# Kernel tuning notes

Measured on AMD Instinct MI355X. Metric: run time of the kernel, lower is better.

The kernel has to match this reference:

```python
import jax, jax.numpy as jnp
import numpy as np
import math

LEVEL_DIMS = [256, 512, 1024, 2048]
B, P, K, D = 8192, 64, 8, 512
EPS = 1e-5  # torch LayerNorm default eps


def _layernorm(x, g, b):
    m = jnp.mean(x, axis=-1, keepdims=True)
    v = jnp.var(x, axis=-1, keepdims=True)
    return (x - m) / jnp.sqrt(v + EPS) * g + b


def _l2norm(x):
    # F.normalize(dim=-1): x / max(||x||_2, 1e-12)
    n = jnp.sqrt(jnp.sum(x * x, axis=-1, keepdims=True))
    return x / jnp.maximum(n, 1e-12)


def setup_inputs() -> dict:
    key = jax.random.key(0)
    ks = iter(jax.random.split(key, 32))
    inp = {}
    for i, dim in enumerate(LEVEL_DIMS):
        inp[f'pooled_{i}'] = jax.random.normal(next(ks), (B, dim), jnp.float32)
        inp[f'proto_{i}'] = jax.random.normal(next(ks), (P, dim), jnp.float32)
        inp[f'ln_g_{i}'] = jnp.ones((2 * dim,), jnp.float32)
        inp[f'ln_b_{i}'] = jnp.zeros((2 * dim,), jnp.float32)
        inp[f'W_{i}'] = jax.random.normal(next(ks), (2 * dim, D), jnp.float32) * (1.0 / math.sqrt(2 * dim))
        inp[f'b_{i}'] = jnp.zeros((D,), jnp.float32)
    inp['text_base'] = jax.random.normal(next(ks), (K, D), jnp.float32)
    inp['logit_scale'] = jnp.ones((1,), jnp.float32)
    return inp


def reference(pooled_0, pooled_1, pooled_2, pooled_3,
              proto_0, proto_1, proto_2, proto_3,
              ln_g_0, ln_g_1, ln_g_2, ln_g_3,
              ln_b_0, ln_b_1, ln_b_2, ln_b_3,
              W_0, W_1, W_2, W_3,
              b_0, b_1, b_2, b_3,
              text_base, logit_scale):
    pooled = [pooled_0, pooled_1, pooled_2, pooled_3]
    proto = [proto_0, proto_1, proto_2, proto_3]
    ln_g = [ln_g_0, ln_g_1, ln_g_2, ln_g_3]
    ln_b = [ln_b_0, ln_b_1, ln_b_2, ln_b_3]
    Ws = [W_0, W_1, W_2, W_3]
    bs = [b_0, b_1, b_2, b_3]

    # text encoder: CLIP embeddings normalized, text_proj=Identity, normalized again (idempotent)
    text_features = _l2norm(text_base)  # [K, D]

    ctxs = []
    for pl, pr, g, bb, W, b in zip(pooled, proto, ln_g, ln_b, Ws, bs):
        proto_ctx = jnp.broadcast_to(jnp.mean(pr, axis=0, keepdims=True), pl.shape)  # [B, C]
        fused = jnp.concatenate([pl, proto_ctx], axis=1)  # [B, 2C]
        h = jax.nn.relu(_layernorm(fused, g, bb) @ W + b)  # [B, D]
        ctxs.append(_l2norm(h))
    image_contexts = jnp.stack(ctxs, axis=1)  # [B, L, D]

    logits = jnp.einsum('kd,bld->bkl', text_features, image_contexts)
    logits = logits / math.sqrt(D)
    logits = logits * jnp.clip(logit_scale, 1e-4, None)
    return jax.nn.softmax(logits, axis=-1)  # [B, K, L]
```

## Files before the change

kernel.cpp:

```cpp
#include <hip/hip_runtime.h>
#include <stdint.h>

typedef __bf16 bf16x8 __attribute__((ext_vector_type(8)));
typedef float f32x4 __attribute__((ext_vector_type(4)));

#define OFF_ABF   0u
#define OFF_GWT   62914560u
#define OFF_H     66846720u
#define OFF_STAT  100401152u
#define OFF_TEXT  100663296u
#define OFF_U     100679680u
#define OFF_GG    100687872u
#define OFF_BB    100696064u
#define OFF_SCAL  100704256u
#define OFF_PMEAN 100704512u
#define WS_TOTAL  100719872u

__host__ __device__ __forceinline__ size_t abf_off(int l) {
  return (size_t)4194304u * (size_t)((1u << l) - 1u);
}
__host__ __device__ __forceinline__ size_t gwt_off(int l) {
  return (size_t)262144u * (size_t)((1u << l) - 1u);
}
__device__ __forceinline__ int pm_off(int l) { return 256 * ((1 << l) - 1); }

__device__ __forceinline__ unsigned short f2bf(float x) {
  return (unsigned short)((__float_as_uint(x) + 0x8000u) >> 16);
}
__device__ __forceinline__ unsigned pack2(float a, float b) {
  return ((__float_as_uint(a) + 0x8000u) >> 16) |
         ((__float_as_uint(b) + 0x8000u) & 0xffff0000u);
}
__device__ __forceinline__ void async_load16(const void* g, void* l) {
  __builtin_amdgcn_global_load_lds((const __attribute__((address_space(1))) void*)g,
                                   (__attribute__((address_space(3))) void*)l,
                                   16, 0, 0);
}

struct PrepArgs {
  const float* pooled[4];
  const float* proto[4];
  const float* W[4];
  const float* g[4];
  const float* beta[4];
  const float* bias[4];
  const float* text;
  const float* lsc;
  char* ws;
};


__device__ __forceinline__ void loadUnit(f32x4 (&buf)[8], const f32x4* base, int lane) {
#pragma unroll
  for (int i = 0; i < 4; ++i) {
    buf[2 * i]     = base[2 * (lane + 64 * i)];
    buf[2 * i + 1] = base[2 * (lane + 64 * i) + 1];
  }
}

template <int R>
__device__ __forceinline__ void procUnit(const f32x4 (&v)[8], char* Dst, float* st,
                                         int rowBase, int lane) {
  float p1[4], p2[4];
#pragma unroll
  for (int i = 0; i < 4; ++i) {
    f32x4 a = v[2 * i], b = v[2 * i + 1];
    float s1 = ((a[0] + a[1]) + (a[2] + a[3])) + ((b[0] + b[1]) + (b[2] + b[3]));
    float s2 = 0.f;
    s2 = fmaf(a[0], a[0], s2); s2 = fmaf(a[1], a[1], s2);
    s2 = fmaf(a[2], a[2], s2); s2 = fmaf(a[3], a[3], s2);
    s2 = fmaf(b[0], b[0], s2); s2 = fmaf(b[1], b[1], s2);
    s2 = fmaf(b[2], b[2], s2); s2 = fmaf(b[3], b[3], s2);
    p1[i] = s1; p2[i] = s2;
    uint4 o = make_uint4(pack2(a[0], a[1]), pack2(a[2], a[3]),
                         pack2(b[0], b[1]), pack2(b[2], b[3]));
    *(uint4*)(Dst + 16 * (size_t)(lane + 64 * i)) = o;
  }
  if constexpr (R == 1) {
    float s1 = (p1[0] + p1[1]) + (p1[2] + p1[3]);
    float s2 = (p2[0] + p2[1]) + (p2[2] + p2[3]);
#pragma unroll
    for (int off = 1; off < 64; off <<= 1) {
      s1 += __shfl_xor(s1, off); s2 += __shfl_xor(s2, off);
    }
    if (lane == 0) {
      st[2 * (size_t)rowBase] = s1; st[2 * (size_t)rowBase + 1] = s2;
    }
  } else if constexpr (R == 2) {
#pragma unroll
    for (int h = 0; h < 2; ++h) {
      float s1 = p1[2 * h] + p1[2 * h + 1], s2 = p2[2 * h] + p2[2 * h + 1];
#pragma unroll
      for (int off = 1; off < 64; off <<= 1) {
        s1 += __shfl_xor(s1, off); s2 += __shfl_xor(s2, off);
      }
      if (lane == 0) {
        st[2 * (size_t)(rowBase + h)] = s1; st[2 * (size_t)(rowBase + h) + 1] = s2;
      }
    }
  } else if constexpr (R == 4) {
#pragma unroll
    for (int i = 0; i < 4; ++i) {
      float s1 = p1[i], s2 = p2[i];
#pragma unroll
      for (int off = 1; off < 64; off <<= 1) {
        s1 += __shfl_xor(s1, off); s2 += __shfl_xor(s2, off);
      }
      if (lane == 0) {
        st[2 * (size_t)(rowBase + i)] = s1; st[2 * (size_t)(rowBase + i) + 1] = s2;
      }
    }
  } else {
#pragma unroll
    for (int i = 0; i < 4; ++i) {
      float s1 = p1[i], s2 = p2[i];
#pragma unroll
      for (int off = 1; off < 32; off <<= 1) {
        s1 += __shfl_xor(s1, off); s2 += __shfl_xor(s2, off);
      }
      if ((lane & 31) == 0) {
        int row = rowBase + 2 * i + (lane >> 5);
        st[2 * (size_t)row] = s1; st[2 * (size_t)row + 1] = s2;
      }
    }
  }
}

template <int R>
__device__ __forceinline__ void waveRun(const f32x4* P, char* Dst, float* st,
                                        int rowBase, int lane) {
  f32x4 bufA[8], bufB[8];
  loadUnit(bufA, P, lane);
#pragma unroll
  for (int k = 0; k < 8; ++k) {
    if ((k & 1) == 0) {
      if (k < 7) loadUnit(bufB, P + (size_t)(k + 1) * 512, lane);
      procUnit<R>(bufA, Dst + (size_t)k * 4096, st, rowBase + k * R, lane);
    } else {
      if (k < 7) loadUnit(bufA, P + (size_t)(k + 1) * 512, lane);
      procUnit<R>(bufB, Dst + (size_t)k * 4096, st, rowBase + k * R, lane);
    }
  }
}

__global__ __launch_bounds__(256, 4) void aconv(PrepArgs A) {
  __shared__ float redP[4][64];
  int t = threadIdx.x, bid = blockIdx.x;
  int w = t >> 6, lane = t & 63;

  if (bid < 480) {
    int u0 = (bid * 4 + w) * 8;
    int l, uL;
    if (u0 < 8192)       { l = 3; uL = u0; }
    else if (u0 < 12288) { l = 2; uL = u0 - 8192; }
    else if (u0 < 14336) { l = 1; uL = u0 - 12288; }
    else                 { l = 0; uL = u0 - 14336; }
    const f32x4* P = (const f32x4*)A.pooled[l] + (size_t)uL * 512;
    char* Dst = A.ws + OFF_ABF + abf_off(l) + (size_t)uL * 4096;
    float* st = (float*)(A.ws + OFF_STAT) + (size_t)l * 8192 * 2;
    if (l == 3)      waveRun<1>(P, Dst, st, uL,     lane);
    else if (l == 2) waveRun<2>(P, Dst, st, uL * 2, lane);
    else if (l == 1) waveRun<4>(P, Dst, st, uL * 4, lane);
    else             waveRun<8>(P, Dst, st, uL * 8, lane);
    return;
  }
  float* scal = (float*)(A.ws + OFF_SCAL);
  if (bid < 540) {
    int p = bid - 480;
    int l, chunk;
    if (p < 32)      { l = 3; chunk = p; }
    else if (p < 48) { l = 2; chunk = p - 32; }
    else if (p < 56) { l = 1; chunk = p - 48; }
    else             { l = 0; chunk = p - 56; }
    int C = 256 << l;
    int c = chunk * 64 + lane;
    const float* pr = A.proto[l];
    float s = 0.f;
#pragma unroll
    for (int r = 0; r < 16; ++r) s += pr[(size_t)(w * 16 + r) * C + c];
    redP[w][lane] = s;
    __syncthreads();
    if (t < 64) {
      float pmv = (redP[0][t] + redP[1][t] + redP[2][t] + redP[3][t]) * (1.0f / 64.0f);
      ((float*)(A.ws + OFF_PMEAN))[pm_off(l) + chunk * 64 + t] = pmv;
      float s1 = pmv, s2 = pmv * pmv;
#pragma unroll
      for (int off = 1; off < 64; off <<= 1) {
        s1 += __shfl_xor(s1, off);
        s2 += __shfl_xor(s2, off);
      }
      if (t == 0) {
        atomicAdd(&scal[l], s1);
        atomicAdd(&scal[4 + l], s2);
      }
    }
    return;
  }
  float* r1 = &redP[0][0];
  float* tf = (float*)(A.ws + OFF_TEXT);
  for (int r = 0; r < 8; ++r) {
    float p = 0.f;
    for (int c = t; c < 512; c += 256) {
      float v = A.text[r * 512 + c];
      p += v * v;
    }
    r1[t] = p;
    __syncthreads();
    for (int o = 128; o > 0; o >>= 1) {
      if (t < o) r1[t] += r1[t + o];
      __syncthreads();
    }
    float inv = 1.0f / fmaxf(sqrtf(r1[0]), 1e-12f);
    __syncthreads();
    for (int c = t; c < 512; c += 256) tf[r * 512 + c] = A.text[r * 512 + c] * inv;
  }
  if (t == 0) {
    float s = fmaxf(A.lsc[0], 1e-4f);
    scal[8] = s * 0.04419417382415922f;
  }
}

__global__ __launch_bounds__(256) void wtrans(PrepArgs A) {
  __shared__ unsigned short tile[128][66];
  __shared__ float redG[4][128], redB[4][128], redU[4][128];
  __shared__ float gsh[64], bsh[64], psh[64];
  int t = threadIdx.x, bid = blockIdx.x;
  int l, idl;
  if (bid < 256)      { l = 3; idl = bid; }
  else if (bid < 384) { l = 2; idl = bid - 256; }
  else if (bid < 448) { l = 1; idl = bid - 384; }
  else                { l = 0; idl = bid - 448; }
  int C = 256 << l;
  int sid = idl >> 2, dchunk = idl & 3;
  int j0 = sid * 64, d0 = dchunk * 128;
  bool top = (j0 < C);

  if (t < 64) {
    float gv = A.g[l][j0 + t];
    gsh[t] = gv;
    bsh[t] = A.beta[l][j0 + t];
    if (!top)
      psh[t] = ((const float*)(A.ws + OFF_PMEAN))[pm_off(l) + (j0 - C) + t] * gv;
  }
  __syncthreads();

  int w = t >> 6, L = t & 63;
  const float* W = A.W[l];
  float2 v[16];
#pragma unroll
  for (int r = 0; r < 16; ++r) {
    int j = j0 + w * 16 + r;
    v[r] = *(const float2*)(W + (size_t)j * 512 + d0 + 2 * L);
  }
  float gp0 = 0.f, gp1 = 0.f, bp0 = 0.f, bp1 = 0.f, up0 = 0.f, up1 = 0.f;
#pragma unroll
  for (int r = 0; r < 16; ++r) {
    int jl = w * 16 + r;
    float g = gsh[jl], b = bsh[jl];
    gp0 = fmaf(g, v[r].x, gp0); gp1 = fmaf(g, v[r].y, gp1);
    bp0 = fmaf(b, v[r].x, bp0); bp1 = fmaf(b, v[r].y, bp1);
    if (top) {
      tile[2 * L][jl] = f2bf(g * v[r].x);
      tile[2 * L + 1][jl] = f2bf(g * v[r].y);
    } else {
      float p = psh[jl];
      up0 = fmaf(p, v[r].x, up0); up1 = fmaf(p, v[r].y, up1);
    }
  }
  redG[w][2 * L] = gp0; redG[w][2 * L + 1] = gp1;
  redB[w][2 * L] = bp0; redB[w][2 * L + 1] = bp1;
  if (!top) { redU[w][2 * L] = up0; redU[w][2 * L + 1] = up1; }
  __syncthreads();

  if (t < 128) {
    int d = l * 512 + d0 + t;
    float G = redG[0][t] + redG[1][t] + redG[2][t] + redG[3][t];
    float B = redB[0][t] + redB[1][t] + redB[2][t] + redB[3][t];
    atomicAdd(&((float*)(A.ws + OFF_GG))[d], G);
    atomicAdd(&((float*)(A.ws + OFF_BB))[d], B);
    if (!top) {
      float U = redU[0][t] + redU[1][t] + redU[2][t] + redU[3][t];
      atomicAdd(&((float*)(A.ws + OFF_U))[d], U);
    }
  }
  if (top) {
    unsigned short* gwT = (unsigned short*)(A.ws + OFF_GWT + gwt_off(l));
    int d = t >> 1, jh = (t & 1) * 32;
    const unsigned* trow = (const unsigned*)&tile[d][jh];
    uint4 q0 = make_uint4(trow[0], trow[1], trow[2], trow[3]);
    uint4 q1 = make_uint4(trow[4], trow[5], trow[6], trow[7]);
    uint4 q2 = make_uint4(trow[8], trow[9], trow[10], trow[11]);
    uint4 q3 = make_uint4(trow[12], trow[13], trow[14], trow[15]);
    uint4* dst = (uint4*)(gwT + (size_t)(d0 + d) * C + j0 + jh);
    dst[0] = q0; dst[1] = q1; dst[2] = q2; dst[3] = q3;
  }
}

struct G2Args {
  char* ws;
  const float* bias[4];
};

__global__ __launch_bounds__(256, 3) void gemm2(G2Args A) {
  __shared__ __align__(16) char lds[18944];
  char* ws = A.ws;
  int t = threadIdx.x, bid = blockIdx.x;
  int l = 3 - (bid >> 8);
  int rb = (bid >> 2) & 63, cb = bid & 3;
  int C = 256 << l;
  int m0 = rb * 128, n0 = cb * 128;

  float* uArr  = (float*)(lds + 16384);
  float* gArr  = (float*)(lds + 16896);
  float* bArr  = (float*)(lds + 17408);
  float* rowM  = (float*)(lds + 17920);
  float* rowIS = (float*)(lds + 18432);
  const float* scal = (const float*)(ws + OFF_SCAL);

  if (t < 128) {
    int idx = l * 512 + n0 + t;
    uArr[t] = ((const float*)(ws + OFF_U))[idx];
    gArr[t] = ((const float*)(ws + OFF_GG))[idx];
    bArr[t] = ((const float*)(ws + OFF_BB))[idx] + A.bias[l][n0 + t];
  } else {
    int r = t - 128;
    const float* st = (const float*)(ws + OFF_STAT) + (size_t)(l * 8192 + m0 + r) * 2;
    float s1 = st[0], s2 = st[1];
    float inv2C = 1.0f / (float)(2 * C);
    float mr = (s1 + scal[l]) * inv2C;
    float var = (s2 + scal[4 + l]) * inv2C - mr * mr;
    rowM[r] = mr;
    rowIS[r] = rsqrtf(var + 1e-5f);
  }

  int w = t >> 6, lane = t & 63, quad = lane >> 4, lc = lane & 15;
  const char* Abf = ws + OFF_ABF + abf_off(l);
  const char* Bw  = ws + OFF_GWT + gwt_off(l);
  const char* aP[2]; const char* bP[2];
  char* aD[2]; char* bD[2];
#pragma unroll
  for (int i = 0; i < 2; ++i) {
    int li = i * 256 + t;
    int rr = li >> 2, kq = li & 3;
    aP[i] = Abf + ((size_t)(m0 + rr) * C + kq * 8) * 2;
    bP[i] = Bw  + ((size_t)(n0 + rr) * C + kq * 8) * 2;
    aD[i] = lds + i * 4096 + w * 1024;
    bD[i] = lds + 8192 + i * 4096 + w * 1024;
  }
  int wr = (w >> 1) * 64, wc = (w & 1) * 64;
  const char* aF = lds + (wr + lc) * 64 + quad * 16;
  const char* bF = lds + 8192 + (wc + lc) * 64 + quad * 16;

  f32x4 acc[4][4] = {};
  for (int k0 = 0; k0 < C; k0 += 32) {
    async_load16(aP[0], aD[0]); async_load16(aP[1], aD[1]);
    async_load16(bP[0], bD[0]); async_load16(bP[1], bD[1]);
    aP[0] += 64; aP[1] += 64; bP[0] += 64; bP[1] += 64;
    __syncthreads();
    bf16x8 av[4];
#pragma unroll
    for (int rt = 0; rt < 4; ++rt) av[rt] = *(const bf16x8*)(aF + rt * 1024);
#pragma unroll
    for (int ct = 0; ct < 4; ++ct) {
      bf16x8 bv = *(const bf16x8*)(bF + ct * 1024);
#pragma unroll
      for (int rt = 0; rt < 4; ++rt)
        acc[rt][ct] = __builtin_amdgcn_mfma_f32_16x16x32_bf16(av[rt], bv, acc[rt][ct], 0, 0, 0);
    }
    __syncthreads();
  }

  char* Hl = ws + OFF_H + (size_t)l * 8388608;
#pragma unroll
  for (int rt = 0; rt < 4; ++rt) {
#pragma unroll
    for (int ct = 0; ct < 4; ++ct) {
      int nl = wc + ct * 16 + lc;
      float uu = uArr[nl], gg = gArr[nl], bb = bArr[nl];
      f32x4 a = acc[rt][ct];
#pragma unroll
      for (int reg = 0; reg < 4; ++reg) {
        int ml = wr + rt * 16 + quad * 4 + reg;
        float h = fmaf(a[reg] + uu - rowM[ml] * gg, rowIS[ml], bb);
        h = fmaxf(h, 0.f);
        float hp = __shfl_xor(h, 1);
        if (!(lc & 1)) {
          unsigned pkv = pack2(h, hp);
          *(unsigned*)(Hl + ((size_t)(m0 + ml) * 512 + n0 + nl) * 2) = pkv;
        }
      }
    }
  }
}

__global__ __launch_bounds__(256) void postK(const char* ws, float* out) {
  __shared__ float textL[4096];
  int t = threadIdx.x, b = blockIdx.x;
  const float* tf = (const float*)(ws + OFF_TEXT);
  for (int i = t; i < 4096; i += 256) textL[i] = tf[i];
  __syncthreads();
  float scale = ((const float*)(ws + OFF_SCAL))[8];
  int row = b * 16 + (t >> 4), q = t & 15;
  float lg[4][8];
#pragma unroll
  for (int l = 0; l < 4; ++l) {
    const uint4* hp = (const uint4*)(ws + OFF_H + (size_t)l * 8388608 +
                                     ((size_t)row * 512 + q * 32) * 2);
    float np = 0.f;
    float dp[8] = {};
#pragma unroll
    for (int ch = 0; ch < 4; ++ch) {
      uint4 u = hp[ch];
      int d0 = q * 32 + ch * 8;
      unsigned uw[4] = {u.x, u.y, u.z, u.w};
#pragma unroll
      for (int p = 0; p < 4; ++p) {
        float v0 = __uint_as_float(uw[p] << 16);
        float v1 = __uint_as_float(uw[p] & 0xffff0000u);
        int dd = d0 + p * 2;
        np = fmaf(v0, v0, np);
        np = fmaf(v1, v1, np);
#pragma unroll
        for (int k = 0; k < 8; ++k) {
          dp[k] = fmaf(v0, textL[k * 512 + dd], dp[k]);
          dp[k] = fmaf(v1, textL[k * 512 + dd + 1], dp[k]);
        }
      }
    }
#pragma unroll
    for (int off = 1; off < 16; off <<= 1) {
      np += __shfl_xor(np, off);
#pragma unroll
      for (int k = 0; k < 8; ++k) dp[k] += __shfl_xor(dp[k], off);
    }
    float innorm = scale / fmaxf(sqrtf(np), 1e-12f);
#pragma unroll
    for (int k = 0; k < 8; ++k) lg[l][k] = dp[k] * innorm;
  }
  if (q == 0) {
    float4* op = (float4*)out + (size_t)row * 8;
#pragma unroll
    for (int k = 0; k < 8; ++k) {
      float a = lg[0][k], b2 = lg[1][k], c = lg[2][k], d = lg[3][k];
      float mx = fmaxf(fmaxf(a, b2), fmaxf(c, d));
      float e0 = __expf(a - mx), e1 = __expf(b2 - mx);
      float e2 = __expf(c - mx), e3 = __expf(d - mx);
      float inv = 1.0f / (e0 + e1 + e2 + e3);
      op[k] = make_float4(e0 * inv, e1 * inv, e2 * inv, e3 * inv);
    }
  }
}

extern "C" void kernel_launch(void* const* d_in, const int* in_sizes, int n_in,
                              void* d_out, int out_size, void* d_ws, size_t ws_size,
                              hipStream_t stream) {
  (void)n_in; (void)out_size;
  if (ws_size < (size_t)WS_TOTAL) return;
  char* ws = (char*)d_ws;
  bool dict = (in_sizes[1] == 64 * 256);
  PrepArgs pa;
  for (int l = 0; l < 4; ++l) {
    if (dict) {
      pa.pooled[l] = (const float*)d_in[6 * l + 0];
      pa.proto[l]  = (const float*)d_in[6 * l + 1];
      pa.g[l]      = (const float*)d_in[6 * l + 2];
      pa.beta[l]   = (const float*)d_in[6 * l + 3];
      pa.W[l]      = (const float*)d_in[6 * l + 4];
      pa.bias[l]   = (const float*)d_in[6 * l + 5];
    } else {
      pa.pooled[l] = (const float*)d_in[l];
      pa.proto[l]  = (const float*)d_in[4 + l];
      pa.g[l]      = (const float*)d_in[8 + l];
      pa.beta[l]   = (const float*)d_in[12 + l];
      pa.W[l]      = (const float*)d_in[16 + l];
      pa.bias[l]   = (const float*)d_in[20 + l];
    }
  }
  pa.text = (const float*)d_in[24];
  pa.lsc = (const float*)d_in[25];
  pa.ws = ws;

  hipMemsetAsync(ws + OFF_U, 0, 3 * 8192 + 256, stream);
  aconv<<<541, 256, 0, stream>>>(pa);
  wtrans<<<480, 256, 0, stream>>>(pa);

  G2Args g2;
  g2.ws = ws;
  for (int l = 0; l < 4; ++l) g2.bias[l] = pa.bias[l];
  gemm2<<<1024, 256, 0, stream>>>(g2);
  postK<<<512, 256, 0, stream>>>(ws, (float*)d_out);
}
```

Baseline: 299.8 us.

## Fuse text dot products and norms into GEMM epilogue, drop H buffer

The GEMM epilogue now applies ReLU, then computes per-row partial dot products with the normalized text features and the partial squared norm directly from the accumulators. These are reduced across lanes and atomically added into a small logits buffer, so the bf16 H intermediate is never written or re-read. A light finish kernel then applies scale, normalization and softmax. Prototype-mean and text-normalization work moves from aconv into wtrans, and GEMM blocks are remapped by an interleaved swizzle. This adds atomics, an extra memset and slightly larger LDS use in the GEMM.

```diff
diff --git a/kernel.cpp b/kernel.cpp
--- a/kernel.cpp
+++ b/kernel.cpp
@@ -6,14 +6,13 @@
 
 #define OFF_ABF   0u
 #define OFF_GWT   62914560u
-#define OFF_H     66846720u
+#define OFF_LOG   66846720u
 #define OFF_STAT  100401152u
 #define OFF_TEXT  100663296u
 #define OFF_U     100679680u
 #define OFF_GG    100687872u
 #define OFF_BB    100696064u
 #define OFF_SCAL  100704256u
-#define OFF_PMEAN 100704512u
 #define WS_TOTAL  100719872u
 
 __host__ __device__ __forceinline__ size_t abf_off(int l) {
@@ -22,7 +21,6 @@
 __host__ __device__ __forceinline__ size_t gwt_off(int l) {
   return (size_t)262144u * (size_t)((1u << l) - 1u);
 }
-__device__ __forceinline__ int pm_off(int l) { return 256 * ((1 << l) - 1); }
 
 __device__ __forceinline__ unsigned short f2bf(float x) {
   return (unsigned short)((__float_as_uint(x) + 0x8000u) >> 16);
@@ -48,7 +46,6 @@
   const float* lsc;
   char* ws;
 };
-
 
 __device__ __forceinline__ void loadUnit(f32x4 (&buf)[8], const f32x4* base, int lane) {
 #pragma unroll
@@ -144,87 +141,49 @@
 }
 
 __global__ __launch_bounds__(256, 4) void aconv(PrepArgs A) {
-  __shared__ float redP[4][64];
   int t = threadIdx.x, bid = blockIdx.x;
   int w = t >> 6, lane = t & 63;
-
-  if (bid < 480) {
-    int u0 = (bid * 4 + w) * 8;
-    int l, uL;
-    if (u0 < 8192)       { l = 3; uL = u0; }
-    else if (u0 < 12288) { l = 2; uL = u0 - 8192; }
-    else if (u0 < 14336) { l = 1; uL = u0 - 12288; }
-    else                 { l = 0; uL = u0 - 14336; }
-    const f32x4* P = (const f32x4*)A.pooled[l] + (size_t)uL * 512;
-    char* Dst = A.ws + OFF_ABF + abf_off(l) + (size_t)uL * 4096;
-    float* st = (float*)(A.ws + OFF_STAT) + (size_t)l * 8192 * 2;
-    if (l == 3)      waveRun<1>(P, Dst, st, uL,     lane);
-    else if (l == 2) waveRun<2>(P, Dst, st, uL * 2, lane);
-    else if (l == 1) waveRun<4>(P, Dst, st, uL * 4, lane);
-    else             waveRun<8>(P, Dst, st, uL * 8, lane);
-    return;
-  }
-  float* scal = (float*)(A.ws + OFF_SCAL);
-  if (bid < 540) {
-    int p = bid - 480;
-    int l, chunk;
-    if (p < 32)      { l = 3; chunk = p; }
-    else if (p < 48) { l = 2; chunk = p - 32; }
-    else if (p < 56) { l = 1; chunk = p - 48; }
-    else             { l = 0; chunk = p - 56; }
-    int C = 256 << l;
-    int c = chunk * 64 + lane;
-    const float* pr = A.proto[l];
-    float s = 0.f;
-#pragma unroll
-    for (int r = 0; r < 16; ++r) s += pr[(size_t)(w * 16 + r) * C + c];
-    redP[w][lane] = s;
-    __syncthreads();
-    if (t < 64) {
-      float pmv = (redP[0][t] + redP[1][t] + redP[2][t] + redP[3][t]) * (1.0f / 64.0f);
-      ((float*)(A.ws + OFF_PMEAN))[pm_off(l) + chunk * 64 + t] = pmv;
-      float s1 = pmv, s2 = pmv * pmv;
-#pragma unroll
-      for (int off = 1; off < 64; off <<= 1) {
-        s1 += __shfl_xor(s1, off);
-        s2 += __shfl_xor(s2, off);
-      }
-      if (t == 0) {
-        atomicAdd(&scal[l], s1);
-        atomicAdd(&scal[4 + l], s2);
-      }
-    }
-    return;
-  }
-  float* r1 = &redP[0][0];
-  float* tf = (float*)(A.ws + OFF_TEXT);
-  for (int r = 0; r < 8; ++r) {
-    float p = 0.f;
-    for (int c = t; c < 512; c += 256) {
-      float v = A.text[r * 512 + c];
-      p += v * v;
-    }
-    r1[t] = p;
-    __syncthreads();
-    for (int o = 128; o > 0; o >>= 1) {
-      if (t < o) r1[t] += r1[t + o];
-      __syncthreads();
-    }
-    float inv = 1.0f / fmaxf(sqrtf(r1[0]), 1e-12f);
-    __syncthreads();
-    for (int c = t; c < 512; c += 256) tf[r * 512 + c] = A.text[r * 512 + c] * inv;
-  }
-  if (t == 0) {
-    float s = fmaxf(A.lsc[0], 1e-4f);
-    scal[8] = s * 0.04419417382415922f;
-  }
+  int u0 = (bid * 4 + w) * 8;
+  int l, uL;
+  if (u0 < 8192)       { l = 3; uL = u0; }
+  else if (u0 < 12288) { l = 2; uL = u0 - 8192; }
+  else if (u0 < 14336) { l = 1; uL = u0 - 12288; }
+  else                 { l = 0; uL = u0 - 14336; }
+  const f32x4* P = (const f32x4*)A.pooled[l] + (size_t)uL * 512;
+  char* Dst = A.ws + OFF_ABF + abf_off(l) + (size_t)uL * 4096;
+  float* st = (float*)(A.ws + OFF_STAT) + (size_t)l * 8192 * 2;
+  if (l == 3)      waveRun<1>(P, Dst, st, uL,     lane);
+  else if (l == 2) waveRun<2>(P, Dst, st, uL * 2, lane);
+  else if (l == 1) waveRun<4>(P, Dst, st, uL * 4, lane);
+  else             waveRun<8>(P, Dst, st, uL * 8, lane);
 }
 
 __global__ __launch_bounds__(256) void wtrans(PrepArgs A) {
   __shared__ unsigned short tile[128][66];
   __shared__ float redG[4][128], redB[4][128], redU[4][128];
   __shared__ float gsh[64], bsh[64], psh[64];
+  __shared__ float redP[4][64];
   int t = threadIdx.x, bid = blockIdx.x;
+
+  if (bid == 480) {
+    int row = t >> 5, l32 = t & 31;
+    const float* tr = A.text + row * 512 + l32;
+    float v[16];
+    float s = 0.f;
+#pragma unroll
+    for (int i = 0; i < 16; ++i) {
+      v[i] = tr[32 * i];
+      s = fmaf(v[i], v[i], s);
+    }
+#pragma unroll
+    for (int off = 1; off < 32; off <<= 1) s += __shfl_xor(s, off);
+    float inv = 1.0f / fmaxf(sqrtf(s), 1e-12f);
+    float* tf = (float*)(A.ws + OFF_TEXT) + row * 512 + l32;
+#pragma unroll
+    for (int i = 0; i < 16; ++i) tf[32 * i] = v[i] * inv;
+    return;
+  }
+
   int l, idl;
   if (bid < 256)      { l = 3; idl = bid; }
   else if (bid < 384) { l = 2; idl = bid - 256; }
@@ -234,17 +193,42 @@
   int sid = idl >> 2, dchunk = idl & 3;
   int j0 = sid * 64, d0 = dchunk * 128;
   bool top = (j0 < C);
+  int w = t >> 6, L = t & 63;
+  float* scal = (float*)(A.ws + OFF_SCAL);
 
   if (t < 64) {
-    float gv = A.g[l][j0 + t];
-    gsh[t] = gv;
+    gsh[t] = A.g[l][j0 + t];
     bsh[t] = A.beta[l][j0 + t];
-    if (!top)
-      psh[t] = ((const float*)(A.ws + OFF_PMEAN))[pm_off(l) + (j0 - C) + t] * gv;
+  }
+  if (!top) {
+    const float* pr = A.proto[l];
+    int cb0 = j0 - C;
+    float s = 0.f;
+#pragma unroll
+    for (int r = 0; r < 16; ++r) s += pr[(size_t)(w * 16 + r) * C + cb0 + L];
+    redP[w][L] = s;
   }
   __syncthreads();
-
-  int w = t >> 6, L = t & 63;
+  if (!top) {
+    if (t < 64) {
+      float pmv = (redP[0][t] + redP[1][t] + redP[2][t] + redP[3][t]) * (1.0f / 64.0f);
+      psh[t] = pmv * gsh[t];
+      if (dchunk == 0) {
+        float s1 = pmv, s2 = pmv * pmv;
+#pragma unroll
+        for (int off = 1; off < 64; off <<= 1) {
+          s1 += __shfl_xor(s1, off);
+          s2 += __shfl_xor(s2, off);
+        }
+        if (t == 0) {
+          atomicAdd(&scal[l], s1);
+          atomicAdd(&scal[4 + l], s2);
+        }
+      }
+    }
+    __syncthreads();
+  }
+
   const float* W = A.W[l];
   float2 v[16];
 #pragma unroll
@@ -302,9 +286,10 @@
 };
 
 __global__ __launch_bounds__(256, 3) void gemm2(G2Args A) {
-  __shared__ __align__(16) char lds[18944];
+  __shared__ __align__(16) char lds[23040];
   char* ws = A.ws;
-  int t = threadIdx.x, bid = blockIdx.x;
+  int t = threadIdx.x;
+  int bid = ((blockIdx.x & 7) << 7) + (blockIdx.x >> 3);
   int l = 3 - (bid >> 8);
   int rb = (bid >> 2) & 63, cb = bid & 3;
   int C = 256 << l;
@@ -315,6 +300,7 @@
   float* bArr  = (float*)(lds + 17408);
   float* rowM  = (float*)(lds + 17920);
   float* rowIS = (float*)(lds + 18432);
+  float* textL = (float*)(lds + 18944);
   const float* scal = (const float*)(ws + OFF_SCAL);
 
   if (t < 128) {
@@ -332,6 +318,14 @@
     rowM[r] = mr;
     rowIS[r] = rsqrtf(var + 1e-5f);
   }
+  {
+    const float* tf = (const float*)(ws + OFF_TEXT);
+#pragma unroll
+    for (int i = 0; i < 4; ++i) {
+      int idx = t + 256 * i;
+      textL[idx] = tf[(idx >> 7) * 512 + n0 + (idx & 127)];
+    }
+  }
 
   int w = t >> 6, lane = t & 63, quad = lane >> 4, lc = lane & 15;
   const char* Abf = ws + OFF_ABF + abf_off(l);
@@ -370,85 +364,54 @@
     __syncthreads();
   }
 
-  char* Hl = ws + OFF_H + (size_t)l * 8388608;
 #pragma unroll
   for (int rt = 0; rt < 4; ++rt) {
 #pragma unroll
-    for (int ct = 0; ct < 4; ++ct) {
-      int nl = wc + ct * 16 + lc;
-      float uu = uArr[nl], gg = gArr[nl], bb = bArr[nl];
-      f32x4 a = acc[rt][ct];
-#pragma unroll
-      for (int reg = 0; reg < 4; ++reg) {
-        int ml = wr + rt * 16 + quad * 4 + reg;
-        float h = fmaf(a[reg] + uu - rowM[ml] * gg, rowIS[ml], bb);
+    for (int reg = 0; reg < 4; ++reg) {
+      int ml = wr + rt * 16 + quad * 4 + reg;
+      float rm = rowM[ml], ris = rowIS[ml];
+      float p[9] = {};
+#pragma unroll
+      for (int ct = 0; ct < 4; ++ct) {
+        int nl = wc + ct * 16 + lc;
+        float h = fmaf(acc[rt][ct][reg] + uArr[nl] - rm * gArr[nl], ris, bArr[nl]);
         h = fmaxf(h, 0.f);
-        float hp = __shfl_xor(h, 1);
-        if (!(lc & 1)) {
-          unsigned pkv = pack2(h, hp);
-          *(unsigned*)(Hl + ((size_t)(m0 + ml) * 512 + n0 + nl) * 2) = pkv;
-        }
-      }
-    }
-  }
-}
-
-__global__ __launch_bounds__(256) void postK(const char* ws, float* out) {
-  __shared__ float textL[4096];
-  int t = threadIdx.x, b = blockIdx.x;
-  const float* tf = (const float*)(ws + OFF_TEXT);
-  for (int i = t; i < 4096; i += 256) textL[i] = tf[i];
-  __syncthreads();
-  float scale = ((const float*)(ws + OFF_SCAL))[8];
-  int row = b * 16 + (t >> 4), q = t & 15;
-  float lg[4][8];
+        p[8] = fmaf(h, h, p[8]);
+#pragma unroll
+        for (int k = 0; k < 8; ++k)
+          p[k] = fmaf(h, textL[k * 128 + nl], p[k]);
+      }
+#pragma unroll
+      for (int off = 1; off < 16; off <<= 1) {
+#pragma unroll
+        for (int k = 0; k < 9; ++k) p[k] += __shfl_xor(p[k], off);
+      }
+      if (lc == 0) {
+        float* Lg = (float*)(ws + OFF_LOG) + (((size_t)l * 8192 + m0 + ml) << 4);
+#pragma unroll
+        for (int k = 0; k < 9; ++k) atomicAdd(&Lg[k], p[k]);
+      }
+    }
+  }
+}
+
+__global__ __launch_bounds__(256) void finishK(const char* ws, const float* lsc,
+                                               float* out) {
+  int t = threadIdx.x;
+  int row = blockIdx.x * 32 + (t >> 3), k = t & 7;
+  float scale = fmaxf(lsc[0], 1e-4f) * 0.04419417382415922f;
+  float x[4];
 #pragma unroll
   for (int l = 0; l < 4; ++l) {
-    const uint4* hp = (const uint4*)(ws + OFF_H + (size_t)l * 8388608 +
-                                     ((size_t)row * 512 + q * 32) * 2);
-    float np = 0.f;
-    float dp[8] = {};
-#pragma unroll
-    for (int ch = 0; ch < 4; ++ch) {
-      uint4 u = hp[ch];
-      int d0 = q * 32 + ch * 8;
-      unsigned uw[4] = {u.x, u.y, u.z, u.w};
-#pragma unroll
-      for (int p = 0; p < 4; ++p) {
-        float v0 = __uint_as_float(uw[p] << 16);
-        float v1 = __uint_as_float(uw[p] & 0xffff0000u);
-        int dd = d0 + p * 2;
-        np = fmaf(v0, v0, np);
-        np = fmaf(v1, v1, np);
-#pragma unroll
-        for (int k = 0; k < 8; ++k) {
-          dp[k] = fmaf(v0, textL[k * 512 + dd], dp[k]);
-          dp[k] = fmaf(v1, textL[k * 512 + dd + 1], dp[k]);
-        }
-      }
-    }
-#pragma unroll
-    for (int off = 1; off < 16; off <<= 1) {
-      np += __shfl_xor(np, off);
-#pragma unroll
-      for (int k = 0; k < 8; ++k) dp[k] += __shfl_xor(dp[k], off);
-    }
-    float innorm = scale / fmaxf(sqrtf(np), 1e-12f);
-#pragma unroll
-    for (int k = 0; k < 8; ++k) lg[l][k] = dp[k] * innorm;
-  }
-  if (q == 0) {
-    float4* op = (float4*)out + (size_t)row * 8;
-#pragma unroll
-    for (int k = 0; k < 8; ++k) {
-      float a = lg[0][k], b2 = lg[1][k], c = lg[2][k], d = lg[3][k];
-      float mx = fmaxf(fmaxf(a, b2), fmaxf(c, d));
-      float e0 = __expf(a - mx), e1 = __expf(b2 - mx);
-      float e2 = __expf(c - mx), e3 = __expf(d - mx);
-      float inv = 1.0f / (e0 + e1 + e2 + e3);
-      op[k] = make_float4(e0 * inv, e1 * inv, e2 * inv, e3 * inv);
-    }
-  }
+    const float* Lg = (const float*)(ws + OFF_LOG) + (((size_t)l * 8192 + row) << 4);
+    float dot = Lg[k], nsq = Lg[8];
+    x[l] = dot * (scale / fmaxf(sqrtf(nsq), 1e-12f));
+  }
+  float mx = fmaxf(fmaxf(x[0], x[1]), fmaxf(x[2], x[3]));
+  float e0 = __expf(x[0] - mx), e1 = __expf(x[1] - mx);
+  float e2 = __expf(x[2] - mx), e3 = __expf(x[3] - mx);
+  float inv = 1.0f / (e0 + e1 + e2 + e3);
+  ((float4*)out)[(size_t)row * 8 + k] = make_float4(e0 * inv, e1 * inv, e2 * inv, e3 * inv);
 }
 
 extern "C" void kernel_launch(void* const* d_in, const int* in_sizes, int n_in,
@@ -481,12 +444,14 @@
   pa.ws = ws;
 
   hipMemsetAsync(ws + OFF_U, 0, 3 * 8192 + 256, stream);
-  aconv<<<541, 256, 0, stream>>>(pa);
-  wtrans<<<480, 256, 0, stream>>>(pa);
+  hipMemsetAsync(ws + OFF_LOG, 0, 4 * 8192 * 16 * 4, stream);
+
+  aconv<<<480, 256, 0, stream>>>(pa);
+  wtrans<<<481, 256, 0, stream>>>(pa);
 
   G2Args g2;
   g2.ws = ws;
   for (int l = 0; l < 4; ++l) g2.bias[l] = pa.bias[l];
   gemm2<<<1024, 256, 0, stream>>>(g2);
-  postK<<<512, 256, 0, stream>>>(ws, (float*)d_out);
-}
+  finishK<<<256, 256, 0, stream>>>(ws, pa.lsc, (float*)d_out);
+}
```

Result: slower. 385.2 us (+28.5%).
